# Performance work log

Measured on AMD Instinct MI355X. Metric: run time of the kernel, lower is better.

Reference implementation:

```python
import jax, jax.numpy as jnp
import numpy as np

B, S, D = 4, 2048, 1024
E, TOP_K = 8, 2
CAPACITY_FACTOR = 1.1
H = 4 * D  # expert hidden dim


def setup_inputs() -> dict:
    key = jax.random.key(0)
    ks = jax.random.split(key, 12)
    sc = 0.02
    return {
        "x": jax.random.normal(ks[0], (B, S, D), jnp.float32),
        "noise": jax.random.normal(ks[1], (B, S, E), jnp.float32),
        "W_route": jax.random.normal(ks[2], (D, E), jnp.float32) * sc,
        "b_route": jnp.zeros((E,), jnp.float32),
        "W_noise": jax.random.normal(ks[3], (D, E), jnp.float32) * sc,
        "b_noise": jnp.zeros((E,), jnp.float32),
        "W1": jax.random.normal(ks[4], (E, D, H), jnp.float32) * sc,
        "b1": jnp.zeros((E, H), jnp.float32),
        "W2": jax.random.normal(ks[5], (E, H, D), jnp.float32) * sc,
        "b2": jnp.zeros((E, D), jnp.float32),
    }


def reference(x, noise, W_route, b_route, W_noise, b_noise, W1, b1, W2, b2):
    # ---- NoisyTopkRouter ----
    logits = x @ W_route + b_route                  # [B,S,E]
    noise_logits = x @ W_noise + b_noise            # [B,S,E]
    noisy = logits + noise * jax.nn.softplus(noise_logits)
    top_vals, top_idx = jax.lax.top_k(noisy, TOP_K)  # [B,S,k]
    probs_k = jax.nn.softmax(top_vals, axis=-1)      # softmax over sparse(-inf elsewhere) == softmax over top-k
    onehot = jax.nn.one_hot(top_idx, E, dtype=x.dtype)          # [B,S,k,E]
    router_probs = jnp.einsum('bske,bsk->bse', onehot, probs_k)  # [B,S,E]
    expert_mask = onehot.sum(axis=-2)                            # [B,S,E] (top_k indices are distinct)
    lb_loss = E * jnp.sum(router_probs.mean(axis=(0, 1)) * expert_mask.mean(axis=(0, 1)))

    # ---- capacity-limited dispatch / expert MLP / combine ----
    T = B * S
    cap = int(T * TOP_K / E * CAPACITY_FACTOR)
    flat_x = x.reshape(T, D)
    flat_gate = router_probs.reshape(T, E)
    mask = expert_mask.reshape(T, E) > 0                         # token selects expert
    pos = jnp.cumsum(mask.astype(jnp.int32), axis=0)             # 1-based slot within expert
    keep = mask & (pos <= cap)                                   # first `cap` tokens per expert (flat order)
    priority = jnp.where(keep, jnp.arange(T)[:, None], T)        # [T,E]
    order = jnp.argsort(priority, axis=0)[:cap]                  # [cap,E] token ids (stable: token order)
    valid = (jnp.take_along_axis(priority, order, axis=0) < T).T  # [E,cap]
    gather_idx = order.T                                         # [E,cap]

    x_e = flat_x[gather_idx]                                     # [E,cap,D]
    h = jax.nn.relu(jnp.einsum('ecd,edh->ech', x_e, W1) + b1[:, None, :])
    out_e = jnp.einsum('ech,ehd->ecd', h, W2) + b2[:, None, :]   # dropout is identity in eval mode
    gate = flat_gate[gather_idx, jnp.arange(E)[:, None]]         # [E,cap]
    weighted = out_e * (gate * valid)[..., None]
    updates = jnp.zeros_like(flat_x).at[gather_idx.reshape(-1)].add(weighted.reshape(-1, D))
    return updates.reshape(B, S, D), lb_loss
```

## Files before the change

### kernel.cpp

```cpp
#include <hip/hip_runtime.h>
#include <hip/hip_bf16.h>

#define D_DIM 1024
#define H_DIM 4096
#define E_NUM 8
#define T_TOK 8192
#define CAPN 2252
#define CAP_PAD 2304
#define MT 18

typedef __attribute__((ext_vector_type(8))) short short8;
typedef __attribute__((ext_vector_type(4))) float f32x4;
typedef __attribute__((ext_vector_type(4))) float f4v;
typedef const __attribute__((address_space(1))) void* gas_ptr;
typedef __attribute__((address_space(3))) void* las_ptr;

__device__ __forceinline__ unsigned short f2bf(float f) {
    __hip_bfloat16 h = __float2bfloat16(f);
    return __builtin_bit_cast(unsigned short, h);
}

__global__ void router_kernel(const float* __restrict__ x,
                              const float* __restrict__ noise,
                              const float* __restrict__ Wr,
                              const float* __restrict__ br,
                              const float* __restrict__ Wn,
                              const float* __restrict__ bn,
                              __hip_bfloat16* __restrict__ xb,
                              int* __restrict__ tok_e,
                              float* __restrict__ tok_g)
{
    const int l = threadIdx.x & 63;
    const int w = threadIdx.x >> 6;
    const int t = blockIdx.x * 4 + w;
    const float* xr = x + (size_t)t * D_DIM;

    float ar[8] = {0,0,0,0,0,0,0,0};
    float an[8] = {0,0,0,0,0,0,0,0};
#pragma unroll
    for (int i = 0; i < 4; ++i) {
        int d = i * 256 + l * 4;
        f4v xv = __builtin_nontemporal_load((const f4v*)(xr + d));
        ushort4 xq;
        xq.x = f2bf(xv.x); xq.y = f2bf(xv.y); xq.z = f2bf(xv.z); xq.w = f2bf(xv.w);
        *(ushort4*)(xb + (size_t)t * D_DIM + d) = xq;
        float xs[4] = {xv.x, xv.y, xv.z, xv.w};
#pragma unroll
        for (int j = 0; j < 4; ++j) {
            const float* wrp = Wr + (size_t)(d + j) * 8;
            float4 wa = *(const float4*)wrp;
            float4 wb = *(const float4*)(wrp + 4);
            ar[0] = fmaf(xs[j], wa.x, ar[0]); ar[1] = fmaf(xs[j], wa.y, ar[1]);
            ar[2] = fmaf(xs[j], wa.z, ar[2]); ar[3] = fmaf(xs[j], wa.w, ar[3]);
            ar[4] = fmaf(xs[j], wb.x, ar[4]); ar[5] = fmaf(xs[j], wb.y, ar[5]);
            ar[6] = fmaf(xs[j], wb.z, ar[6]); ar[7] = fmaf(xs[j], wb.w, ar[7]);
            const float* wnp = Wn + (size_t)(d + j) * 8;
            float4 na = *(const float4*)wnp;
            float4 nb = *(const float4*)(wnp + 4);
            an[0] = fmaf(xs[j], na.x, an[0]); an[1] = fmaf(xs[j], na.y, an[1]);
            an[2] = fmaf(xs[j], na.z, an[2]); an[3] = fmaf(xs[j], na.w, an[3]);
            an[4] = fmaf(xs[j], nb.x, an[4]); an[5] = fmaf(xs[j], nb.y, an[5]);
            an[6] = fmaf(xs[j], nb.z, an[6]); an[7] = fmaf(xs[j], nb.w, an[7]);
        }
    }
#pragma unroll
    for (int e = 0; e < 8; ++e) {
#pragma unroll
        for (int s = 32; s > 0; s >>= 1) {
            ar[e] += __shfl_xor(ar[e], s, 64);
            an[e] += __shfl_xor(an[e], s, 64);
        }
    }
    if (l == 0) {
        float nv[8];
#pragma unroll
        for (int e = 0; e < 8; ++e) {
            float z = an[e] + bn[e];
            float sp = fmaxf(z, 0.f) + log1pf(expf(-fabsf(z)));
            nv[e] = ar[e] + br[e] + noise[(size_t)t * 8 + e] * sp;
        }
        int e0 = 0; float v0 = nv[0];
#pragma unroll
        for (int e = 1; e < 8; ++e) if (nv[e] > v0) { v0 = nv[e]; e0 = e; }
        int e1 = -1; float v1 = -3.4e38f;
#pragma unroll
        for (int e = 0; e < 8; ++e) if (e != e0 && nv[e] > v1) { v1 = nv[e]; e1 = e; }
        float ex = expf(v1 - v0);
        float p0 = 1.f / (1.f + ex);
        float p1 = ex * p0;
        tok_e[2 * t]     = e0; tok_e[2 * t + 1] = e1;
        tok_g[2 * t]     = p0; tok_g[2 * t + 1] = p1;
    }
}

__global__ void scan_kernel(const int* __restrict__ tok_e,
                            const float* __restrict__ tok_g,
                            int* __restrict__ routed,
                            int* __restrict__ inv,
                            int* __restrict__ nkept,
                            float* __restrict__ lb_out)
{
    const int e = threadIdx.x >> 6;
    const int l = threadIdx.x & 63;
    __shared__ float s_g[E_NUM];
    __shared__ int   s_c[E_NUM];

    int run = 0;
    float gsum = 0.f;
    for (int b = 0; b < 8; ++b) {
        int2  ev[16];
        float2 gv[16];
#pragma unroll
        for (int c = 0; c < 16; ++c) {
            int t = (b * 16 + c) * 64 + l;
            ev[c] = ((const int2*)tok_e)[t];
            gv[c] = ((const float2*)tok_g)[t];
        }
#pragma unroll
        for (int c = 0; c < 16; ++c) {
            int t = (b * 16 + c) * 64 + l;
            int j = (ev[c].x == e) ? 0 : ((ev[c].y == e) ? 1 : -1);
            bool sel = (j >= 0);
            unsigned long long m = __ballot(sel);
            if (sel) {
                int pos = run + __popcll(m & ((1ull << l) - 1ull));
                if (pos < CAPN) {
                    routed[e * CAP_PAD + pos] = t;
                    inv[2 * t + j] = e * CAP_PAD + pos;
                }
                gsum += (j == 0) ? gv[c].x : gv[c].y;
            }
            run += __popcll(m);
        }
    }
#pragma unroll
    for (int s = 32; s > 0; s >>= 1) gsum += __shfl_xor(gsum, s, 64);
    int nk = min(run, CAPN);
    for (int s = nk + l; s < CAP_PAD; s += 64) routed[e * CAP_PAD + s] = 0;
    if (l == 0) { nkept[e] = nk; s_g[e] = gsum; s_c[e] = run; }
    __syncthreads();
    if (threadIdx.x == 0) {
        float lb = 0.f;
        for (int ee = 0; ee < E_NUM; ++ee)
            lb += (s_g[ee] / (float)T_TOK) * ((float)s_c[ee] / (float)T_TOK);
        lb_out[0] = lb * (float)E_NUM;
    }
}

__global__ void gather_kernel(const ushort* __restrict__ xb,
                              const int* __restrict__ routed,
                              ushort* __restrict__ xg)
{
    const int dc = blockIdx.x & 127;
    const int e  = blockIdx.x >> 7;
    ushort* dst = xg + (size_t)(e * 128 + dc) * CAP_PAD * 8;
    const int* rte = routed + e * CAP_PAD;
#pragma unroll
    for (int p = 0; p < 9; ++p) {
        int m = p * 256 + threadIdx.x;
        int tok = rte[m];
        ulonglong2 v = *(const ulonglong2*)(xb + (size_t)tok * D_DIM + dc * 8);
        *(ulonglong2*)(dst + (size_t)m * 8) = v;
    }
}

__global__ void chunk_weights(const float* __restrict__ in,
                              ushort* __restrict__ out,
                              int K, int N)
{
    __shared__ float tile[64][65];
    const int e = blockIdx.z;
    const int k0 = blockIdx.y * 64, n0 = blockIdx.x * 64;
    const float* src = in + (size_t)e * K * N;
    ushort* dst = out + (size_t)e * (K / 8) * N * 8;
    const int t = threadIdx.x;
    const int rr = t >> 4, c4 = (t & 15) * 4;
#pragma unroll
    for (int p = 0; p < 4; ++p) {
        int r = p * 16 + rr;
        f4v v = __builtin_nontemporal_load(
            (const f4v*)(src + (size_t)(k0 + r) * N + n0 + c4));
        tile[r][c4]     = v.x; tile[r][c4 + 1] = v.y;
        tile[r][c4 + 2] = v.z; tile[r][c4 + 3] = v.w;
    }
    __syncthreads();
    const int n = t & 63, kc = t >> 6;
#pragma unroll
    for (int p = 0; p < 2; ++p) {
        int kcc = p * 4 + kc;
        ushort g[8];
#pragma unroll
        for (int j = 0; j < 8; ++j) g[j] = f2bf(tile[kcc * 8 + j][n]);
        *(short8*)(dst + ((size_t)(k0 / 8 + kcc) * N + n0 + n) * 8) = *(const short8*)g;
    }
}

template <int MODE>
__global__ __launch_bounds__(256, 3) void ffn_gemm(
    const ushort* __restrict__ A,
    const ushort* __restrict__ Bt,
    const float* __restrict__ bias,
    const int* __restrict__ nkept,
    ushort* __restrict__ outH,
    float*  __restrict__ outP,
    int sshift, int nkt)
{
    constexpr int KD = (MODE == 1) ? D_DIM : H_DIM;
    constexpr int ND = (MODE == 1) ? H_DIM : D_DIM;
    constexpr int NC = KD / 8;
    __shared__ ushort lds[24576];

    unsigned total = gridDim.x * gridDim.y * gridDim.z;
    unsigned flat  = blockIdx.x + gridDim.x * (blockIdx.y + gridDim.y * blockIdx.z);
    unsigned sw    = (flat & 7) * (total >> 3) + (flat >> 3);
    unsigned bnL   = sw & 7;
    unsigned r1    = sw >> 3;
    unsigned bm    = r1 % gridDim.y;
    unsigned r2    = r1 / gridDim.y;
    unsigned ng    = gridDim.x >> 3;
    unsigned bn    = (r2 % ng) * 8 + bnL;
    unsigned bz    = r2 / ng;

    const int e  = (int)(bz >> sshift);
    const int sp = (int)(bz & ((1u << sshift) - 1u));
    const int m0 = (int)bm * 128, n0 = (int)bn * 128;
    if (m0 >= nkept[e]) return;
    const int kc0 = sp * (nkt << 2);

    const int tid  = threadIdx.x;
    const int lane = tid & 63;
    const int w    = tid >> 6;
    const int chi  = w >> 1;
    const int rhE  = (w & 1) * 64;
    const int rhB  = (w & 1) * 1024;

    const size_t sAc = (size_t)CAP_PAD * 8;
    const size_t sBc = (size_t)ND * 8;
    const size_t tsA = 4 * sAc;
    const size_t tsB = 4 * sBc;

    const ushort* Ab = A  + ((size_t)e * NC * CAP_PAD + (size_t)(m0 + rhE + lane)) * 8
                          + (size_t)kc0 * sAc;
    const ushort* Bb = Bt + ((size_t)e * NC * ND + (size_t)(n0 + rhE + lane)) * 8
                          + (size_t)kc0 * sBc;
    const ushort* A0 = Ab + (size_t)chi * sAc;
    const ushort* A2 = Ab + (size_t)(2 + chi) * sAc;
    const ushort* B0 = Bb + (size_t)chi * sBc;
    const ushort* B2 = Bb + (size_t)(2 + chi) * sBc;

    auto gl = [&](const ushort* g, int ldsbyte) {
        __builtin_amdgcn_global_load_lds((gas_ptr)g, (las_ptr)((char*)lds + ldsbyte), 16, 0, 0);
    };
    auto issueA = [&](size_t off, int stB) {
        gl(A0 + off, stB + chi * 2048 + rhB);
        gl(A2 + off, stB + (2 + chi) * 2048 + rhB);
    };
    auto issueB = [&](size_t off, int stB) {
        gl(B0 + off, stB + 8192 + chi * 2048 + rhB);
        gl(B2 + off, stB + 8192 + (2 + chi) * 2048 + rhB);
    };

    issueA(0, 0);        issueB(0, 0);
    issueA(tsA, 16384);  issueB(tsB, 16384);
    asm volatile("s_waitcnt vmcnt(4)" ::: "memory");
    __builtin_amdgcn_s_barrier();

    f32x4 acc[4][4] = {};
    const int wm = (w >> 1) * 64;
    const int wn = (w & 1) * 64;
    const int fr = lane & 15;
    const int fq = lane >> 4;

    int rdS = 0;
    int wrB = 32768;
    size_t oA = 2 * tsA;
    size_t oB = 2 * tsB;

    for (int kt = 0; kt < nkt; ++kt) {
        const ushort* Ard = lds + rdS;
        const ushort* Brd = Ard + 4096;

        short8 af[4], bfr[4];
#pragma unroll
        for (int j = 0; j < 4; ++j)
            bfr[j] = *(const short8*)(Brd + fq * 1024 + (wn + j * 16 + fr) * 8);
#pragma unroll
        for (int i = 0; i < 4; ++i)
            af[i] = *(const short8*)(Ard + fq * 1024 + (wm + i * 16 + fr) * 8);

        issueA(oA, wrB);
        issueB(oB, wrB);

        __builtin_amdgcn_s_setprio(1);
#pragma unroll
        for (int i = 0; i < 4; ++i)
#pragma unroll
            for (int j = 0; j < 4; ++j)
                acc[i][j] = __builtin_amdgcn_mfma_f32_16x16x32_bf16(af[i], bfr[j], acc[i][j], 0, 0, 0);
        __builtin_amdgcn_s_setprio(0);

        asm volatile("s_waitcnt vmcnt(4)" ::: "memory");
        __builtin_amdgcn_s_barrier();

        rdS = (rdS == 16384) ? 0 : rdS + 8192;
        wrB = (wrB == 32768) ? 0 : wrB + 16384;
        if (kt < nkt - 3) { oA += tsA; oB += tsB; }
    }

#pragma unroll
    for (int j = 0; j < 4; ++j) {
        int nc = n0 + wn + j * 16 + fr;
        float bv = (MODE == 1) ? bias[e * ND + nc] : 0.f;
#pragma unroll
        for (int i = 0; i < 4; ++i) {
            int mr = m0 + wm + i * 16 + (fq << 2);
#pragma unroll
            for (int r = 0; r < 4; ++r) {
                float v = acc[i][j][r] + bv;
                if (MODE == 1) {
                    v = fmaxf(v, 0.f);
                    outH[(((size_t)e * 512 + (nc >> 3)) * CAP_PAD + mr + r) * 8 + (nc & 7)] = f2bf(v);
                } else {
                    outP[((size_t)(sp * E_NUM + e) * CAP_PAD + mr + r) * D_DIM + nc] = v;
                }
            }
        }
    }
}

__global__ void combine_kernel(const float* __restrict__ part,
                               const int* __restrict__ inv,
                               const float* __restrict__ tok_g,
                               const float* __restrict__ b2,
                               int S,
                               float* __restrict__ out)
{
    const int t = blockIdx.x;
    const int d = threadIdx.x * 4;
    f4v r = {0.f, 0.f, 0.f, 0.f};
#pragma unroll
    for (int j = 0; j < 2; ++j) {
        int i = inv[2 * t + j];
        if (i >= 0) {
            float g = tok_g[2 * t + j];
            int e = i / CAP_PAD;
            f4v a = *(const f4v*)(b2 + (size_t)e * D_DIM + d);
            for (int s = 0; s < S; ++s) {
                f4v p = __builtin_nontemporal_load(
                    (const f4v*)(part + ((size_t)s * E_NUM * CAP_PAD + i) * D_DIM + d));
                a += p;
            }
            r += g * a;
        }
    }
    __builtin_nontemporal_store(r, (f4v*)(out + (size_t)t * D_DIM + d));
}

extern "C" void kernel_launch(void* const* d_in, const int* in_sizes, int n_in,
                              void* d_out, int out_size, void* d_ws, size_t ws_size,
                              hipStream_t stream)
{
    const float* x  = (const float*)d_in[0];
    const float* nz = (const float*)d_in[1];
    const float* Wr = (const float*)d_in[2];
    const float* br = (const float*)d_in[3];
    const float* Wn = (const float*)d_in[4];
    const float* bn = (const float*)d_in[5];
    const float* W1 = (const float*)d_in[6];
    const float* b1 = (const float*)d_in[7];
    const float* W2 = (const float*)d_in[8];
    const float* b2 = (const float*)d_in[9];
    float* out = (float*)d_out;
    char* ws = (char*)d_ws;

    const size_t sz_w2c = (size_t)E_NUM * (H_DIM / 8) * D_DIM * 8 * 2;
    const size_t sz_h   = (size_t)E_NUM * 512 * CAP_PAD * 8 * 2;
    const size_t o_w2c  = 0;
    const size_t o_h    = o_w2c + sz_w2c;
    const size_t o_sm   = o_h + sz_h;
    const size_t o_dyn  = o_sm + (1u << 20);
    const size_t sz_xg  = (size_t)E_NUM * 128 * CAP_PAD * 8 * 2;
    const size_t sz_xb  = (size_t)T_TOK * D_DIM * 2;
    const size_t sz_w1c = (size_t)E_NUM * (D_DIM / 8) * H_DIM * 8 * 2;
    const size_t sz_p1  = sz_xg + sz_xb + sz_w1c;
    const size_t sz_part1 = (size_t)E_NUM * CAP_PAD * D_DIM * 4;

    int sshift = 1;
    while (sshift > 0) {
        size_t need = o_dyn + ((sz_part1 << sshift) > sz_p1 ? (sz_part1 << sshift) : sz_p1);
        if (need <= ws_size) break;
        --sshift;
    }
    const int S = 1 << sshift;

    ushort* w2c  = (ushort*)(ws + o_w2c);
    ushort* hbuf = (ushort*)(ws + o_h);
    int*    rt   = (int*)(ws + o_sm);
    int*    te   = (int*)(ws + o_sm + 131072);
    float*  tg   = (float*)(ws + o_sm + 262144);
    int*    inv  = (int*)(ws + o_sm + 393216);
    int*    nk   = (int*)(ws + o_sm + 524288);
    ushort* xg   = (ushort*)(ws + o_dyn);
    ushort* xb   = (ushort*)(ws + o_dyn + sz_xg);
    ushort* w1c  = (ushort*)(ws + o_dyn + sz_xg + sz_xb);
    float*  part = (float*)(ws + o_dyn);

    (void)hipMemsetAsync(inv, 0xFF, (size_t)T_TOK * 2 * 4, stream);

    router_kernel<<<T_TOK / 4, 256, 0, stream>>>(x, nz, Wr, br, Wn, bn,
                                                 (__hip_bfloat16*)xb, te, tg);
    scan_kernel<<<1, 512, 0, stream>>>(te, tg, rt, inv, nk, out + (size_t)T_TOK * D_DIM);
    chunk_weights<<<dim3(D_DIM / 64, H_DIM / 64, E_NUM), 256, 0, stream>>>(W2, w2c, H_DIM, D_DIM);
    chunk_weights<<<dim3(H_DIM / 64, D_DIM / 64, E_NUM), 256, 0, stream>>>(W1, w1c, D_DIM, H_DIM);
    gather_kernel<<<E_NUM * 128, 256, 0, stream>>>(xb, rt, xg);

    ffn_gemm<1><<<dim3(H_DIM / 128, MT, E_NUM), 256, 0, stream>>>(
        xg, w1c, b1, nk, hbuf, nullptr, 0, D_DIM / 32);

    ffn_gemm<2><<<dim3(D_DIM / 128, MT, E_NUM << sshift), 256, 0, stream>>>(
        hbuf, w2c, nullptr, nk, nullptr, part, sshift, (H_DIM / 32) >> sshift);

    combine_kernel<<<T_TOK, 256, 0, stream>>>(part, inv, tg, b2, S, out);
}
```

Baseline: 575.2 us.

## Fuse router and weight-chunking into one prep kernel, simplify GEMM tile swizzle

Merges the router kernel and both weight conversion/chunking kernels into a single launch that picks its role from the block index. This removes two kernel launches and lets the memory-bound weight conversion overlap with router work instead of running back to back. Separately, the GEMM block remapping drops the 8-wide N-group swizzle in favour of a plain N-fastest decomposition, which changes L2 reuse patterns. The shared-memory tile is now allocated for router blocks too, which may slightly lower their occupancy.

```diff
diff --git a/kernel.cpp b/kernel.cpp
--- a/kernel.cpp
+++ b/kernel.cpp
@@ -20,76 +20,119 @@
     return __builtin_bit_cast(unsigned short, h);
 }
 
-__global__ void router_kernel(const float* __restrict__ x,
-                              const float* __restrict__ noise,
-                              const float* __restrict__ Wr,
-                              const float* __restrict__ br,
-                              const float* __restrict__ Wn,
-                              const float* __restrict__ bn,
-                              __hip_bfloat16* __restrict__ xb,
-                              int* __restrict__ tok_e,
-                              float* __restrict__ tok_g)
-{
-    const int l = threadIdx.x & 63;
-    const int w = threadIdx.x >> 6;
-    const int t = blockIdx.x * 4 + w;
-    const float* xr = x + (size_t)t * D_DIM;
-
-    float ar[8] = {0,0,0,0,0,0,0,0};
-    float an[8] = {0,0,0,0,0,0,0,0};
-#pragma unroll
-    for (int i = 0; i < 4; ++i) {
-        int d = i * 256 + l * 4;
-        f4v xv = __builtin_nontemporal_load((const f4v*)(xr + d));
-        ushort4 xq;
-        xq.x = f2bf(xv.x); xq.y = f2bf(xv.y); xq.z = f2bf(xv.z); xq.w = f2bf(xv.w);
-        *(ushort4*)(xb + (size_t)t * D_DIM + d) = xq;
-        float xs[4] = {xv.x, xv.y, xv.z, xv.w};
-#pragma unroll
-        for (int j = 0; j < 4; ++j) {
-            const float* wrp = Wr + (size_t)(d + j) * 8;
-            float4 wa = *(const float4*)wrp;
-            float4 wb = *(const float4*)(wrp + 4);
-            ar[0] = fmaf(xs[j], wa.x, ar[0]); ar[1] = fmaf(xs[j], wa.y, ar[1]);
-            ar[2] = fmaf(xs[j], wa.z, ar[2]); ar[3] = fmaf(xs[j], wa.w, ar[3]);
-            ar[4] = fmaf(xs[j], wb.x, ar[4]); ar[5] = fmaf(xs[j], wb.y, ar[5]);
-            ar[6] = fmaf(xs[j], wb.z, ar[6]); ar[7] = fmaf(xs[j], wb.w, ar[7]);
-            const float* wnp = Wn + (size_t)(d + j) * 8;
-            float4 na = *(const float4*)wnp;
-            float4 nb = *(const float4*)(wnp + 4);
-            an[0] = fmaf(xs[j], na.x, an[0]); an[1] = fmaf(xs[j], na.y, an[1]);
-            an[2] = fmaf(xs[j], na.z, an[2]); an[3] = fmaf(xs[j], na.w, an[3]);
-            an[4] = fmaf(xs[j], nb.x, an[4]); an[5] = fmaf(xs[j], nb.y, an[5]);
-            an[6] = fmaf(xs[j], nb.z, an[6]); an[7] = fmaf(xs[j], nb.w, an[7]);
-        }
-    }
-#pragma unroll
-    for (int e = 0; e < 8; ++e) {
-#pragma unroll
-        for (int s = 32; s > 0; s >>= 1) {
-            ar[e] += __shfl_xor(ar[e], s, 64);
-            an[e] += __shfl_xor(an[e], s, 64);
-        }
-    }
-    if (l == 0) {
-        float nv[8];
+__global__ __launch_bounds__(256) void prep_kernel(
+    const float* __restrict__ x,
+    const float* __restrict__ noise,
+    const float* __restrict__ Wr,
+    const float* __restrict__ br,
+    const float* __restrict__ Wn,
+    const float* __restrict__ bn,
+    __hip_bfloat16* __restrict__ xb,
+    int* __restrict__ tok_e,
+    float* __restrict__ tok_g,
+    const float* __restrict__ W1,
+    const float* __restrict__ W2,
+    ushort* __restrict__ w1c,
+    ushort* __restrict__ w2c)
+{
+    __shared__ float tile[64][65];
+    const unsigned blk = blockIdx.x;
+
+    if (blk < 2048) {
+        const int l = threadIdx.x & 63;
+        const int w = threadIdx.x >> 6;
+        const int t = blk * 4 + w;
+        const float* xr = x + (size_t)t * D_DIM;
+
+        float ar[8] = {0,0,0,0,0,0,0,0};
+        float an[8] = {0,0,0,0,0,0,0,0};
+#pragma unroll
+        for (int i = 0; i < 4; ++i) {
+            int d = i * 256 + l * 4;
+            f4v xv = __builtin_nontemporal_load((const f4v*)(xr + d));
+            ushort4 xq;
+            xq.x = f2bf(xv.x); xq.y = f2bf(xv.y); xq.z = f2bf(xv.z); xq.w = f2bf(xv.w);
+            *(ushort4*)(xb + (size_t)t * D_DIM + d) = xq;
+            float xs[4] = {xv.x, xv.y, xv.z, xv.w};
+#pragma unroll
+            for (int j = 0; j < 4; ++j) {
+                const float* wrp = Wr + (size_t)(d + j) * 8;
+                float4 wa = *(const float4*)wrp;
+                float4 wb = *(const float4*)(wrp + 4);
+                ar[0] = fmaf(xs[j], wa.x, ar[0]); ar[1] = fmaf(xs[j], wa.y, ar[1]);
+                ar[2] = fmaf(xs[j], wa.z, ar[2]); ar[3] = fmaf(xs[j], wa.w, ar[3]);
+                ar[4] = fmaf(xs[j], wb.x, ar[4]); ar[5] = fmaf(xs[j], wb.y, ar[5]);
+                ar[6] = fmaf(xs[j], wb.z, ar[6]); ar[7] = fmaf(xs[j], wb.w, ar[7]);
+                const float* wnp = Wn + (size_t)(d + j) * 8;
+                float4 na = *(const float4*)wnp;
+                float4 nb = *(const float4*)(wnp + 4);
+                an[0] = fmaf(xs[j], na.x, an[0]); an[1] = fmaf(xs[j], na.y, an[1]);
+                an[2] = fmaf(xs[j], na.z, an[2]); an[3] = fmaf(xs[j], na.w, an[3]);
+                an[4] = fmaf(xs[j], nb.x, an[4]); an[5] = fmaf(xs[j], nb.y, an[5]);
+                an[6] = fmaf(xs[j], nb.z, an[6]); an[7] = fmaf(xs[j], nb.w, an[7]);
+            }
+        }
 #pragma unroll
         for (int e = 0; e < 8; ++e) {
-            float z = an[e] + bn[e];
-            float sp = fmaxf(z, 0.f) + log1pf(expf(-fabsf(z)));
-            nv[e] = ar[e] + br[e] + noise[(size_t)t * 8 + e] * sp;
-        }
-        int e0 = 0; float v0 = nv[0];
-#pragma unroll
-        for (int e = 1; e < 8; ++e) if (nv[e] > v0) { v0 = nv[e]; e0 = e; }
-        int e1 = -1; float v1 = -3.4e38f;
-#pragma unroll
-        for (int e = 0; e < 8; ++e) if (e != e0 && nv[e] > v1) { v1 = nv[e]; e1 = e; }
-        float ex = expf(v1 - v0);
-        float p0 = 1.f / (1.f + ex);
-        float p1 = ex * p0;
-        tok_e[2 * t]     = e0; tok_e[2 * t + 1] = e1;
-        tok_g[2 * t]     = p0; tok_g[2 * t + 1] = p1;
+#pragma unroll
+            for (int s = 32; s > 0; s >>= 1) {
+                ar[e] += __shfl_xor(ar[e], s, 64);
+                an[e] += __shfl_xor(an[e], s, 64);
+            }
+        }
+        if (l == 0) {
+            float nv[8];
+#pragma unroll
+            for (int e = 0; e < 8; ++e) {
+                float z = an[e] + bn[e];
+                float sp = fmaxf(z, 0.f) + log1pf(expf(-fabsf(z)));
+                nv[e] = ar[e] + br[e] + noise[(size_t)t * 8 + e] * sp;
+            }
+            int e0 = 0; float v0 = nv[0];
+#pragma unroll
+            for (int e = 1; e < 8; ++e) if (nv[e] > v0) { v0 = nv[e]; e0 = e; }
+            int e1 = -1; float v1 = -3.4e38f;
+#pragma unroll
+            for (int e = 0; e < 8; ++e) if (e != e0 && nv[e] > v1) { v1 = nv[e]; e1 = e; }
+            float ex = expf(v1 - v0);
+            float p0 = 1.f / (1.f + ex);
+            float p1 = ex * p0;
+            tok_e[2 * t]     = e0; tok_e[2 * t + 1] = e1;
+            tok_g[2 * t]     = p0; tok_g[2 * t + 1] = p1;
+        }
+        return;
+    }
+
+    const float* src; ushort* dstb; int K, N; unsigned i;
+    if (blk < 2048 + 8192) { i = blk - 2048;  K = H_DIM; N = D_DIM; src = W2; dstb = w2c; }
+    else                   { i = blk - 10240; K = D_DIM; N = H_DIM; src = W1; dstb = w1c; }
+    const int nx = N >> 6;
+    const int bx = i % nx;
+    const unsigned rem = i / nx;
+    const int by = rem % (K >> 6);
+    const int e  = rem / (K >> 6);
+    const int k0 = by * 64, n0 = bx * 64;
+    const float* s = src + (size_t)e * K * N;
+    ushort* dst = dstb + (size_t)e * (K / 8) * N * 8;
+    const int t = threadIdx.x;
+    const int rr = t >> 4, c4 = (t & 15) * 4;
+#pragma unroll
+    for (int p = 0; p < 4; ++p) {
+        int r = p * 16 + rr;
+        f4v v = __builtin_nontemporal_load(
+            (const f4v*)(s + (size_t)(k0 + r) * N + n0 + c4));
+        tile[r][c4]     = v.x; tile[r][c4 + 1] = v.y;
+        tile[r][c4 + 2] = v.z; tile[r][c4 + 3] = v.w;
+    }
+    __syncthreads();
+    const int n = t & 63, kc = t >> 6;
+#pragma unroll
+    for (int p = 0; p < 2; ++p) {
+        int kcc = p * 4 + kc;
+        ushort g[8];
+#pragma unroll
+        for (int j = 0; j < 8; ++j) g[j] = f2bf(tile[kcc * 8 + j][n]);
+        *(short8*)(dst + ((size_t)(k0 / 8 + kcc) * N + n0 + n) * 8) = *(const short8*)g;
     }
 }
 
@@ -164,37 +207,6 @@
     }
 }
 
-__global__ void chunk_weights(const float* __restrict__ in,
-                              ushort* __restrict__ out,
-                              int K, int N)
-{
-    __shared__ float tile[64][65];
-    const int e = blockIdx.z;
-    const int k0 = blockIdx.y * 64, n0 = blockIdx.x * 64;
-    const float* src = in + (size_t)e * K * N;
-    ushort* dst = out + (size_t)e * (K / 8) * N * 8;
-    const int t = threadIdx.x;
-    const int rr = t >> 4, c4 = (t & 15) * 4;
-#pragma unroll
-    for (int p = 0; p < 4; ++p) {
-        int r = p * 16 + rr;
-        f4v v = __builtin_nontemporal_load(
-            (const f4v*)(src + (size_t)(k0 + r) * N + n0 + c4));
-        tile[r][c4]     = v.x; tile[r][c4 + 1] = v.y;
-        tile[r][c4 + 2] = v.z; tile[r][c4 + 3] = v.w;
-    }
-    __syncthreads();
-    const int n = t & 63, kc = t >> 6;
-#pragma unroll
-    for (int p = 0; p < 2; ++p) {
-        int kcc = p * 4 + kc;
-        ushort g[8];
-#pragma unroll
-        for (int j = 0; j < 8; ++j) g[j] = f2bf(tile[kcc * 8 + j][n]);
-        *(short8*)(dst + ((size_t)(k0 / 8 + kcc) * N + n0 + n) * 8) = *(const short8*)g;
-    }
-}
-
 template <int MODE>
 __global__ __launch_bounds__(256, 3) void ffn_gemm(
     const ushort* __restrict__ A,
@@ -213,13 +225,10 @@
     unsigned total = gridDim.x * gridDim.y * gridDim.z;
     unsigned flat  = blockIdx.x + gridDim.x * (blockIdx.y + gridDim.y * blockIdx.z);
     unsigned sw    = (flat & 7) * (total >> 3) + (flat >> 3);
-    unsigned bnL   = sw & 7;
-    unsigned r1    = sw >> 3;
-    unsigned bm    = r1 % gridDim.y;
-    unsigned r2    = r1 / gridDim.y;
-    unsigned ng    = gridDim.x >> 3;
-    unsigned bn    = (r2 % ng) * 8 + bnL;
-    unsigned bz    = r2 / ng;
+    unsigned bn    = sw % gridDim.x;
+    unsigned t1    = sw / gridDim.x;
+    unsigned bm    = t1 % gridDim.y;
+    unsigned bz    = t1 / gridDim.y;
 
     const int e  = (int)(bz >> sshift);
     const int sp = (int)(bz & ((1u << sshift) - 1u));
@@ -407,11 +416,10 @@
 
     (void)hipMemsetAsync(inv, 0xFF, (size_t)T_TOK * 2 * 4, stream);
 
-    router_kernel<<<T_TOK / 4, 256, 0, stream>>>(x, nz, Wr, br, Wn, bn,
-                                                 (__hip_bfloat16*)xb, te, tg);
+    prep_kernel<<<2048 + 2 * 8192, 256, 0, stream>>>(
+        x, nz, Wr, br, Wn, bn, (__hip_bfloat16*)xb, te, tg, W1, W2, w1c, w2c);
+
     scan_kernel<<<1, 512, 0, stream>>>(te, tg, rt, inv, nk, out + (size_t)T_TOK * D_DIM);
-    chunk_weights<<<dim3(D_DIM / 64, H_DIM / 64, E_NUM), 256, 0, stream>>>(W2, w2c, H_DIM, D_DIM);
-    chunk_weights<<<dim3(H_DIM / 64, D_DIM / 64, E_NUM), 256, 0, stream>>>(W1, w1c, D_DIM, H_DIM);
     gather_kernel<<<E_NUM * 128, 256, 0, stream>>>(xb, rt, xg);
 
     ffn_gemm<1><<<dim3(H_DIM / 128, MT, E_NUM), 256, 0, stream>>>(
```

New measurement: 584.8 us. No clear change (+1.7%).

## Enlarge FFN GEMM block tile to 256x128 with 8x4 MFMA per wave

Applied to the files above, without the earlier changes.

The expert GEMM block tile grows from 128x128 to 256x128, so each wave now computes a 128x64 sub-tile with twice as many accumulators. The LDS staging and async global-to-LDS load mapping are redone to match: 4 A loads and 2 B loads per thread per stage, with larger triple-buffer offsets. Block swizzling is simplified, MT is halved, and launch bounds drop to 2 blocks per SIMD. The aim is higher arithmetic intensity and less B-tile reloading, at the cost of more registers and LDS and therefore lower occupancy.

```diff
diff --git a/kernel.cpp b/kernel.cpp
--- a/kernel.cpp
+++ b/kernel.cpp
@@ -7,7 +7,7 @@
 #define T_TOK 8192
 #define CAPN 2252
 #define CAP_PAD 2304
-#define MT 18
+#define MT 9
 
 typedef __attribute__((ext_vector_type(8))) short short8;
 typedef __attribute__((ext_vector_type(4))) float f32x4;
@@ -196,7 +196,7 @@
 }
 
 template <int MODE>
-__global__ __launch_bounds__(256, 3) void ffn_gemm(
+__global__ __launch_bounds__(256, 2) void ffn_gemm(
     const ushort* __restrict__ A,
     const ushort* __restrict__ Bt,
     const float* __restrict__ bias,
@@ -208,102 +208,97 @@
     constexpr int KD = (MODE == 1) ? D_DIM : H_DIM;
     constexpr int ND = (MODE == 1) ? H_DIM : D_DIM;
     constexpr int NC = KD / 8;
-    __shared__ ushort lds[24576];
+    __shared__ ushort lds[36864];
 
     unsigned total = gridDim.x * gridDim.y * gridDim.z;
     unsigned flat  = blockIdx.x + gridDim.x * (blockIdx.y + gridDim.y * blockIdx.z);
     unsigned sw    = (flat & 7) * (total >> 3) + (flat >> 3);
-    unsigned bnL   = sw & 7;
-    unsigned r1    = sw >> 3;
-    unsigned bm    = r1 % gridDim.y;
-    unsigned r2    = r1 / gridDim.y;
-    unsigned ng    = gridDim.x >> 3;
-    unsigned bn    = (r2 % ng) * 8 + bnL;
-    unsigned bz    = r2 / ng;
+    unsigned bn    = sw % gridDim.x;
+    unsigned t1    = sw / gridDim.x;
+    unsigned bm    = t1 % gridDim.y;
+    unsigned bz    = t1 / gridDim.y;
 
     const int e  = (int)(bz >> sshift);
     const int sp = (int)(bz & ((1u << sshift) - 1u));
-    const int m0 = (int)bm * 128, n0 = (int)bn * 128;
+    const int m0 = (int)bm * 256, n0 = (int)bn * 128;
     if (m0 >= nkept[e]) return;
     const int kc0 = sp * (nkt << 2);
 
     const int tid  = threadIdx.x;
     const int lane = tid & 63;
     const int w    = tid >> 6;
-    const int chi  = w >> 1;
-    const int rhE  = (w & 1) * 64;
-    const int rhB  = (w & 1) * 1024;
+    const int aw   = w << 10;
+    const int bci  = tid >> 7;
+    const int bw   = (w & 1) << 10;
 
     const size_t sAc = (size_t)CAP_PAD * 8;
     const size_t sBc = (size_t)ND * 8;
     const size_t tsA = 4 * sAc;
     const size_t tsB = 4 * sBc;
 
-    const ushort* Ab = A  + ((size_t)e * NC * CAP_PAD + (size_t)(m0 + rhE + lane)) * 8
+    const ushort* Ae = A  + ((size_t)e * NC * CAP_PAD + (size_t)(m0 + tid)) * 8
                           + (size_t)kc0 * sAc;
-    const ushort* Bb = Bt + ((size_t)e * NC * ND + (size_t)(n0 + rhE + lane)) * 8
-                          + (size_t)kc0 * sBc;
-    const ushort* A0 = Ab + (size_t)chi * sAc;
-    const ushort* A2 = Ab + (size_t)(2 + chi) * sAc;
-    const ushort* B0 = Bb + (size_t)chi * sBc;
-    const ushort* B2 = Bb + (size_t)(2 + chi) * sBc;
+    const ushort* Be = Bt + ((size_t)e * NC * ND + (size_t)(n0 + (tid & 127))) * 8
+                          + (size_t)(kc0 + bci) * sBc;
 
     auto gl = [&](const ushort* g, int ldsbyte) {
         __builtin_amdgcn_global_load_lds((gas_ptr)g, (las_ptr)((char*)lds + ldsbyte), 16, 0, 0);
     };
     auto issueA = [&](size_t off, int stB) {
-        gl(A0 + off, stB + chi * 2048 + rhB);
-        gl(A2 + off, stB + (2 + chi) * 2048 + rhB);
+        gl(Ae + off,            stB + 0 * 4096 + aw);
+        gl(Ae + off + sAc,      stB + 1 * 4096 + aw);
+        gl(Ae + off + 2 * sAc,  stB + 2 * 4096 + aw);
+        gl(Ae + off + 3 * sAc,  stB + 3 * 4096 + aw);
     };
     auto issueB = [&](size_t off, int stB) {
-        gl(B0 + off, stB + 8192 + chi * 2048 + rhB);
-        gl(B2 + off, stB + 8192 + (2 + chi) * 2048 + rhB);
+        gl(Be + off,            stB + 16384 + (0 + bci) * 2048 + bw);
+        gl(Be + off + 2 * sBc,  stB + 16384 + (2 + bci) * 2048 + bw);
     };
 
     issueA(0, 0);        issueB(0, 0);
-    issueA(tsA, 16384);  issueB(tsB, 16384);
-    asm volatile("s_waitcnt vmcnt(4)" ::: "memory");
+    issueA(tsA, 24576);  issueB(tsB, 24576);
+    asm volatile("s_waitcnt vmcnt(6)" ::: "memory");
     __builtin_amdgcn_s_barrier();
 
-    f32x4 acc[4][4] = {};
-    const int wm = (w >> 1) * 64;
+    f32x4 acc[8][4] = {};
+    const int wm = (w >> 1) * 128;
     const int wn = (w & 1) * 64;
     const int fr = lane & 15;
     const int fq = lane >> 4;
 
     int rdS = 0;
-    int wrB = 32768;
+    int wrB = 49152;
     size_t oA = 2 * tsA;
     size_t oB = 2 * tsB;
 
     for (int kt = 0; kt < nkt; ++kt) {
         const ushort* Ard = lds + rdS;
-        const ushort* Brd = Ard + 4096;
-
-        short8 af[4], bfr[4];
+        const ushort* Brd = lds + rdS + 8192;
+
+        short8 af[8], bfr[4];
 #pragma unroll
         for (int j = 0; j < 4; ++j)
             bfr[j] = *(const short8*)(Brd + fq * 1024 + (wn + j * 16 + fr) * 8);
 #pragma unroll
-        for (int i = 0; i < 4; ++i)
-            af[i] = *(const short8*)(Ard + fq * 1024 + (wm + i * 16 + fr) * 8);
+        for (int i = 0; i < 8; ++i)
+            af[i] = *(const short8*)(Ard + fq * 2048 + (wm + i * 16 + fr) * 8);
 
         issueA(oA, wrB);
         issueB(oB, wrB);
 
         __builtin_amdgcn_s_setprio(1);
 #pragma unroll
-        for (int i = 0; i < 4; ++i)
+        for (int i = 0; i < 8; ++i)
 #pragma unroll
             for (int j = 0; j < 4; ++j)
                 acc[i][j] = __builtin_amdgcn_mfma_f32_16x16x32_bf16(af[i], bfr[j], acc[i][j], 0, 0, 0);
         __builtin_amdgcn_s_setprio(0);
 
-        asm volatile("s_waitcnt vmcnt(4)" ::: "memory");
+        asm volatile("s_waitcnt vmcnt(6)" ::: "memory");
         __builtin_amdgcn_s_barrier();
 
-        rdS = (rdS == 16384) ? 0 : rdS + 8192;
-        wrB = (wrB == 32768) ? 0 : wrB + 16384;
+        rdS = (rdS == 24576) ? 0 : rdS + 12288;
+        wrB = (wrB == 49152) ? 0 : wrB + 24576;
         if (kt < nkt - 3) { oA += tsA; oB += tsB; }
     }
 
@@ -312,7 +307,7 @@
         int nc = n0 + wn + j * 16 + fr;
         float bv = (MODE == 1) ? bias[e * ND + nc] : 0.f;
 #pragma unroll
-        for (int i = 0; i < 4; ++i) {
+        for (int i = 0; i < 8; ++i) {
             int mr = m0 + wm + i * 16 + (fq << 2);
 #pragma unroll
             for (int r = 0; r < 4; ++r) {
```

Measured after the change: 564.8 us. Within noise of the previous version (-1.8%).
